# Optimization experiments

Measured on AMD Instinct MI355X. Metric: run time of the kernel, lower is better.

Reference implementation:

```python
import jax, jax.numpy as jnp
import numpy as np

N = 4096        # nodes (cells)
E = 131072      # edges (avg degree 32)
IN = 3000       # input features (genes)
HID = 128       # hidden dim per head
H = 4           # attention heads
LAT = 16        # latent dim
NEG_SLOPE = 0.2 # PyG GATConv leaky_relu slope


def _gat_sparse(x, src, dst, W, a_src, a_dst, b, concat):
    """PyG GATConv on an edge list (src -> dst, softmax grouped by dst)."""
    n = x.shape[0]
    h_, c = a_src.shape
    h = (x @ W).reshape(n, h_, c)                      # [N,H,C]
    e_src = (h * a_src[None]).sum(-1)                  # [N,H]
    e_dst = (h * a_dst[None]).sum(-1)                  # [N,H]
    e = jax.nn.leaky_relu(e_src[src] + e_dst[dst], NEG_SLOPE)  # [E,H]
    m = jax.ops.segment_max(e, dst, num_segments=n)
    ex = jnp.exp(e - m[dst])
    denom = jax.ops.segment_sum(ex, dst, num_segments=n)
    alpha = ex / (denom[dst] + 1e-16)                  # PyG softmax eps
    out = jax.ops.segment_sum(alpha[:, :, None] * h[src], dst, num_segments=n)
    out = out.reshape(n, h_ * c) if concat else out.mean(1)
    return out + b


def _gat_dense(x, W, a_src, a_dst, b, concat):
    """GATConv over the complete graph (the SVD low-rank reconstruction is
    generically fully dense, so to_sparse() keeps all N^2 entries; with
    used_edge_weight=False only the structure matters)."""
    n = x.shape[0]
    h_, c = a_src.shape
    h = (x @ W).reshape(n, h_, c)
    e_src = (h * a_src[None]).sum(-1)                  # [N,H]
    e_dst = (h * a_dst[None]).sum(-1)                  # [N,H]
    # scores[i (target), j (source), head]
    scores = jax.nn.leaky_relu(e_dst[:, None, :] + e_src[None, :, :], NEG_SLOPE)
    alpha = jax.nn.softmax(scores, axis=1)             # softmax over sources
    out = jnp.einsum('ijh,jhc->ihc', alpha, h)
    out = out.reshape(n, h_ * c) if concat else out.mean(1)
    return out + b


def setup_inputs() -> dict:
    key = jax.random.key(0)
    ks = jax.random.split(key, 16)
    s = 0.05
    x = jax.random.normal(ks[0], (N, IN), jnp.float32)
    src = jax.random.randint(ks[1], (E,), 0, N, jnp.int32)
    off = jax.random.randint(ks[2], (E,), 1, N, jnp.int32)
    dst = (src + off) % N                              # no self loops (PyG re-adds them)
    edge_index = jnp.stack([src, dst], axis=0)
    edge_attr = jax.random.uniform(ks[3], (E,), jnp.float32)
    D1 = H * HID
    return {
        'x': x, 'edge_index': edge_index, 'edge_attr': edge_attr,
        'W1': jax.random.normal(ks[4], (IN, D1), jnp.float32) * s,
        'a1_src': jax.random.normal(ks[5], (H, HID), jnp.float32) * s,
        'a1_dst': jax.random.normal(ks[6], (H, HID), jnp.float32) * s,
        'b1': jnp.zeros((D1,), jnp.float32),
        'Wm': jax.random.normal(ks[7], (D1, H * LAT), jnp.float32) * s,
        'am_src': jax.random.normal(ks[8], (H, LAT), jnp.float32) * s,
        'am_dst': jax.random.normal(ks[9], (H, LAT), jnp.float32) * s,
        'bm': jnp.zeros((LAT,), jnp.float32),
        'Ws': jax.random.normal(ks[10], (D1, H * LAT), jnp.float32) * s,
        'as_src': jax.random.normal(ks[11], (H, LAT), jnp.float32) * s,
        'as_dst': jax.random.normal(ks[12], (H, LAT), jnp.float32) * s,
        'bs': jnp.zeros((LAT,), jnp.float32),
    }


def reference(x, edge_index, edge_attr, W1, a1_src, a1_dst, b1,
              Wm, am_src, am_dst, bm, Ws, as_src, as_dst, bs):
    loops = jnp.arange(N, dtype=edge_index.dtype)
    src = jnp.concatenate([edge_index[0], loops])      # GATConv add_self_loops=True
    dst = jnp.concatenate([edge_index[1], loops])
    # branch 1: original sparse graph
    x1 = _gat_sparse(x, src, dst, W1, a1_src, a1_dst, b1, True)
    z_mean1 = _gat_sparse(x1, src, dst, Wm, am_src, am_dst, bm, False)
    z_log_std1 = _gat_sparse(x1, src, dst, Ws, as_src, as_dst, bs, False)
    # branch 2: SVD low-rank reconstructed adjacency => complete graph
    x2 = _gat_dense(x, W1, a1_src, a1_dst, b1, True)
    z_mean2 = _gat_dense(x2, Wm, am_src, am_dst, bm, False)
    z_log_std2 = _gat_dense(x2, Ws, as_src, as_dst, bs, False)
    return (z_mean1, z_log_std1, z_mean2, z_log_std2)
```

## Files before the change

kernel.cpp:

```cpp
#include <hip/hip_runtime.h>

typedef unsigned short u16;
typedef unsigned long long u64;
typedef __attribute__((ext_vector_type(8))) short short8;
typedef __attribute__((ext_vector_type(4))) float f32x4;

#define NN   4096
#define EE   131072
#define ETOT (EE + NN)
#define HH   4
#define IND  3000
#define KP   3008
#define D1   512
#define C1   128
#define C2   16

__device__ __forceinline__ float b2f(u16 u){
  union { unsigned int i; float f; } v; v.i = ((unsigned int)u) << 16; return v.f;
}
__device__ __forceinline__ u16 f2b(float f){
  unsigned int x = __float_as_uint(f);
  unsigned int r = (x + 0x7fffu + ((x >> 16) & 1u)) >> 16;
  return (u16)r;
}
__device__ __forceinline__ float lrelu(float x){ return x > 0.f ? x : 0.2f * x; }

__device__ __forceinline__ void glds16(const void* g, void* l){
  __builtin_amdgcn_global_load_lds(
      (const __attribute__((address_space(1))) unsigned int*)g,
      (__attribute__((address_space(3))) unsigned int*)l, 16, 0, 0);
}

__global__ void zero_out_kernel(float* p, int n){
  int i = blockIdx.x * blockDim.x + threadIdx.x;
  if (i < n) p[i] = 0.f;
}

__global__ __launch_bounds__(256) void cvtXW_kernel(const float* __restrict__ X,
    const float* __restrict__ W, u16* __restrict__ Xhi, u16* __restrict__ Xlo,
    u16* __restrict__ Whi, u16* __restrict__ Wlo){
  __shared__ float T[64][65];
  int b = blockIdx.x;
  if (b < 6016){
    int id = b * 256 + threadIdx.x;
    int m = id / 376, ch = id - m * 376;
    int k = ch * 8;
    float v[8];
    if (k + 8 <= IND){
      float4 a = *(const float4*)(X + (size_t)m * IND + k);
      float4 bb = *(const float4*)(X + (size_t)m * IND + k + 4);
      v[0]=a.x; v[1]=a.y; v[2]=a.z; v[3]=a.w; v[4]=bb.x; v[5]=bb.y; v[6]=bb.z; v[7]=bb.w;
    } else {
      #pragma unroll
      for (int j = 0; j < 8; ++j){ int kk = k + j; v[j] = (kk < IND) ? X[(size_t)m*IND + kk] : 0.f; }
    }
    u16 h8[8], l8[8];
    #pragma unroll
    for (int j = 0; j < 8; ++j){ h8[j] = f2b(v[j]); l8[j] = f2b(v[j] - b2f(h8[j])); }
    *(uint4*)(Xhi + (size_t)m * KP + k) = *(uint4*)h8;
    *(uint4*)(Xlo + (size_t)m * KP + k) = *(uint4*)l8;
  } else {
    int wb = b - 6016;
    int kb = wb % 47, nb = wb / 47;
    int k0 = kb * 64, n0 = nb * 64;
    int t = threadIdx.x;
    #pragma unroll
    for (int rr = 0; rr < 4; ++rr){
      int kl = (t >> 4) + rr * 16;
      int nn = (t & 15) * 4;
      int k = k0 + kl;
      float4 v = make_float4(0.f, 0.f, 0.f, 0.f);
      if (k < IND) v = *(const float4*)(W + (size_t)k * D1 + n0 + nn);
      T[kl][nn] = v.x; T[kl][nn+1] = v.y; T[kl][nn+2] = v.z; T[kl][nn+3] = v.w;
    }
    __syncthreads();
    int nloc = t >> 2, kseg = (t & 3) * 16;
    int n = n0 + nloc;
    #pragma unroll
    for (int c2 = 0; c2 < 2; ++c2){
      int kloc = kseg + c2 * 8;
      u16 h8[8], l8[8];
      #pragma unroll
      for (int j = 0; j < 8; ++j){
        float f = T[kloc + j][nloc];
        h8[j] = f2b(f); l8[j] = f2b(f - b2f(h8[j]));
      }
      *(uint4*)(Whi + (size_t)n * KP + k0 + kloc) = *(uint4*)h8;
      *(uint4*)(Wlo + (size_t)n * KP + k0 + kloc) = *(uint4*)l8;
    }
  }
}

__global__ __launch_bounds__(256) void cvtW2_kernel(const float* __restrict__ WM,
    const float* __restrict__ WS, u16* __restrict__ Wh, u16* __restrict__ Wl){
  __shared__ float T[64][65];
  int half = blockIdx.y;
  int k0 = blockIdx.x * 64;
  const float* W = half ? WS : WM;
  int t = threadIdx.x;
  #pragma unroll
  for (int p = 0; p < 4; ++p){
    int r = p * 16 + (t >> 4), c4 = (t & 15) * 4;
    float4 v = *(const float4*)(W + (size_t)(k0 + r) * 64 + c4);
    T[r][c4] = v.x; T[r][c4+1] = v.y; T[r][c4+2] = v.z; T[r][c4+3] = v.w;
  }
  __syncthreads();
  #pragma unroll
  for (int p = 0; p < 4; ++p){
    int n = p * 16 + (t >> 4), k4 = (t & 15) * 4;
    u16 h4[4], l4[4];
    #pragma unroll
    for (int j = 0; j < 4; ++j){
      float f = T[k4 + j][n];
      h4[j] = f2b(f); l4[j] = f2b(f - b2f(h4[j]));
    }
    size_t o = (size_t)(half * 64 + n) * 512 + k0 + k4;
    *(ushort4*)(Wh + o) = *(ushort4*)h4;
    *(ushort4*)(Wl + o) = *(ushort4*)l4;
  }
}

__global__ __launch_bounds__(256) void gemm_mfma(const u16* __restrict__ Xhi,
    const u16* __restrict__ Xlo, const u16* __restrict__ Whi, const u16* __restrict__ Wlo,
    float* __restrict__ Hh){
  __shared__ u16 sAh[64*64], sAl[64*64], sBh[64*64], sBl[64*64];
  int t = threadIdx.x, lane = t & 63;
  int wv = __builtin_amdgcn_readfirstlane(t >> 6);
  int wr = wv >> 1, wc = wv & 1;
  int bm = blockIdx.x * 64, bn = blockIdx.y * 64;
  f32x4 acc[2][2] = {};
  int r0 = t >> 3,         c0 = (t & 7) ^ (r0 & 7);
  int r1 = 32 + (t >> 3),  c1 = (t & 7) ^ (r1 & 7);
  const char* gAh0 = (const char*)(Xhi + (size_t)(bm + r0) * KP) + c0 * 16;
  const char* gAl0 = (const char*)(Xlo + (size_t)(bm + r0) * KP) + c0 * 16;
  const char* gAh1 = (const char*)(Xhi + (size_t)(bm + r1) * KP) + c1 * 16;
  const char* gAl1 = (const char*)(Xlo + (size_t)(bm + r1) * KP) + c1 * 16;
  const char* gBh0 = (const char*)(Whi + (size_t)(bn + r0) * KP) + c0 * 16;
  const char* gBl0 = (const char*)(Wlo + (size_t)(bn + r0) * KP) + c0 * 16;
  const char* gBh1 = (const char*)(Whi + (size_t)(bn + r1) * KP) + c1 * 16;
  const char* gBl1 = (const char*)(Wlo + (size_t)(bn + r1) * KP) + c1 * 16;
  char* lA0 = (char*)0 + t * 16;
  char* lA1 = (char*)0 + (t + 256) * 16;
  int r16 = lane & 15, kq = lane >> 4;
  int aoff[2][2], boff[2][2];
  #pragma unroll
  for (int m = 0; m < 2; ++m)
    #pragma unroll
    for (int ks = 0; ks < 2; ++ks){
      int arow = wr * 32 + m * 16 + r16;
      int cc = ks * 4 + kq;
      aoff[m][ks] = arow * 128 + ((cc ^ (arow & 7)) * 16);
    }
  #pragma unroll
  for (int n = 0; n < 2; ++n)
    #pragma unroll
    for (int ks = 0; ks < 2; ++ks){
      int brow = wc * 32 + n * 16 + r16;
      int cc = ks * 4 + kq;
      boff[n][ks] = brow * 128 + ((cc ^ (brow & 7)) * 16);
    }
  for (int kb = 0; kb < KP * 2; kb += 128){
    glds16(gAh0 + kb, (char*)sAh + (size_t)lA0);
    glds16(gAh1 + kb, (char*)sAh + (size_t)lA1);
    glds16(gAl0 + kb, (char*)sAl + (size_t)lA0);
    glds16(gAl1 + kb, (char*)sAl + (size_t)lA1);
    glds16(gBh0 + kb, (char*)sBh + (size_t)lA0);
    glds16(gBh1 + kb, (char*)sBh + (size_t)lA1);
    glds16(gBl0 + kb, (char*)sBl + (size_t)lA0);
    glds16(gBl1 + kb, (char*)sBl + (size_t)lA1);
    __syncthreads();
    #pragma unroll
    for (int ks = 0; ks < 2; ++ks){
      short8 ah[2], al[2], bh[2], bl[2];
      #pragma unroll
      for (int m = 0; m < 2; ++m){
        ah[m] = *(const short8*)((const char*)sAh + aoff[m][ks]);
        al[m] = *(const short8*)((const char*)sAl + aoff[m][ks]);
      }
      #pragma unroll
      for (int n = 0; n < 2; ++n){
        bh[n] = *(const short8*)((const char*)sBh + boff[n][ks]);
        bl[n] = *(const short8*)((const char*)sBl + boff[n][ks]);
      }
      #pragma unroll
      for (int m = 0; m < 2; ++m)
        #pragma unroll
        for (int n = 0; n < 2; ++n){
          acc[m][n] = __builtin_amdgcn_mfma_f32_16x16x32_bf16(ah[m], bh[n], acc[m][n], 0, 0, 0);
          acc[m][n] = __builtin_amdgcn_mfma_f32_16x16x32_bf16(ah[m], bl[n], acc[m][n], 0, 0, 0);
          acc[m][n] = __builtin_amdgcn_mfma_f32_16x16x32_bf16(al[m], bh[n], acc[m][n], 0, 0, 0);
        }
    }
    __syncthreads();
  }
  #pragma unroll
  for (int m = 0; m < 2; ++m)
    #pragma unroll
    for (int n = 0; n < 2; ++n){
      int row = bm + wr * 32 + m * 16 + kq * 4;
      int col = bn + wc * 32 + n * 16 + r16;
      float* o = Hh + (size_t)row * D1 + col;
      #pragma unroll
      for (int r = 0; r < 4; ++r) o[(size_t)r * D1] = acc[m][n][r];
    }
}

__global__ __launch_bounds__(256) void gemm_h_split(const float* __restrict__ X,
    const float* __restrict__ Wc, float* __restrict__ Hh){
  __shared__ u16 Ahs[64][40], Als[64][40], Bhs[64][40], Bls[64][40];
  int t = threadIdx.x, lane = t & 63, wave = t >> 6;
  int wr = wave >> 1, wcc = wave & 1;
  int bm = blockIdx.x * 64, bn = blockIdx.y * 64;
  f32x4 acc[2][2] = {};
  int arow = t >> 2, akc = (t & 3) << 3;
  int brow = t >> 3, bnc = (t & 7) << 3;
  for (int k0 = 0; k0 < IND; k0 += 32){
    float va[8];
    size_t abase = (size_t)(bm + arow) * IND + k0 + akc;
    if (k0 + akc + 8 <= IND){
      float4 r0 = *(const float4*)(X + abase);
      float4 r1 = *(const float4*)(X + abase + 4);
      va[0]=r0.x; va[1]=r0.y; va[2]=r0.z; va[3]=r0.w;
      va[4]=r1.x; va[5]=r1.y; va[6]=r1.z; va[7]=r1.w;
    } else {
      #pragma unroll
      for (int j = 0; j < 8; ++j){
        int k = k0 + akc + j;
        va[j] = (k < IND) ? X[abase + j] : 0.f;
      }
    }
    #pragma unroll
    for (int j = 0; j < 8; ++j){
      u16 hb = f2b(va[j]);
      Ahs[arow][akc + j] = hb;
      Als[arow][akc + j] = f2b(va[j] - b2f(hb));
    }
    {
      int gk = k0 + brow;
      float vb[8];
      if (gk < IND){
        const float* wp = Wc + (size_t)gk * D1 + bn + bnc;
        float4 r0 = *(const float4*)wp;
        float4 r1 = *(const float4*)(wp + 4);
        vb[0]=r0.x; vb[1]=r0.y; vb[2]=r0.z; vb[3]=r0.w;
        vb[4]=r1.x; vb[5]=r1.y; vb[6]=r1.z; vb[7]=r1.w;
      } else {
        #pragma unroll
        for (int j = 0; j < 8; ++j) vb[j] = 0.f;
      }
      #pragma unroll
      for (int j = 0; j < 8; ++j){
        u16 hb = f2b(vb[j]);
        Bhs[bnc + j][brow] = hb;
        Bls[bnc + j][brow] = f2b(vb[j] - b2f(hb));
      }
    }
    __syncthreads();
    int r16 = lane & 15, kq = (lane >> 4) << 3;
    short8 a0h = *(const short8*)&Ahs[wr*32      + r16][kq];
    short8 a1h = *(const short8*)&Ahs[wr*32 + 16 + r16][kq];
    short8 a0l = *(const short8*)&Als[wr*32      + r16][kq];
    short8 a1l = *(const short8*)&Als[wr*32 + 16 + r16][kq];
    short8 b0h = *(const short8*)&Bhs[wcc*32      + r16][kq];
    short8 b1h = *(const short8*)&Bhs[wcc*32 + 16 + r16][kq];
    short8 b0l = *(const short8*)&Bls[wcc*32      + r16][kq];
    short8 b1l = *(const short8*)&Bls[wcc*32 + 16 + r16][kq];
    acc[0][0] = __builtin_amdgcn_mfma_f32_16x16x32_bf16(a0h, b0h, acc[0][0], 0, 0, 0);
    acc[0][1] = __builtin_amdgcn_mfma_f32_16x16x32_bf16(a0h, b1h, acc[0][1], 0, 0, 0);
    acc[1][0] = __builtin_amdgcn_mfma_f32_16x16x32_bf16(a1h, b0h, acc[1][0], 0, 0, 0);
    acc[1][1] = __builtin_amdgcn_mfma_f32_16x16x32_bf16(a1h, b1h, acc[1][1], 0, 0, 0);
    acc[0][0] = __builtin_amdgcn_mfma_f32_16x16x32_bf16(a0h, b0l, acc[0][0], 0, 0, 0);
    acc[0][1] = __builtin_amdgcn_mfma_f32_16x16x32_bf16(a0h, b1l, acc[0][1], 0, 0, 0);
    acc[1][0] = __builtin_amdgcn_mfma_f32_16x16x32_bf16(a1h, b0l, acc[1][0], 0, 0, 0);
    acc[1][1] = __builtin_amdgcn_mfma_f32_16x16x32_bf16(a1h, b1l, acc[1][1], 0, 0, 0);
    acc[0][0] = __builtin_amdgcn_mfma_f32_16x16x32_bf16(a0l, b0h, acc[0][0], 0, 0, 0);
    acc[0][1] = __builtin_amdgcn_mfma_f32_16x16x32_bf16(a0l, b1h, acc[0][1], 0, 0, 0);
    acc[1][0] = __builtin_amdgcn_mfma_f32_16x16x32_bf16(a1l, b0h, acc[1][0], 0, 0, 0);
    acc[1][1] = __builtin_amdgcn_mfma_f32_16x16x32_bf16(a1l, b1h, acc[1][1], 0, 0, 0);
    __syncthreads();
  }
  int cr = (lane >> 4) << 2, cc = lane & 15;
  for (int i = 0; i < 2; ++i) for (int j = 0; j < 2; ++j){
    int row = bm + wr*32 + i*16 + cr;
    int col = bn + wcc*32 + j*16 + cc;
    float* o = Hh + (size_t)row * D1 + col;
    for (int r = 0; r < 4; ++r) o[(size_t)r * D1] = acc[i][j][r];
  }
}

__global__ __launch_bounds__(256) void transpose_h(const float* __restrict__ h,
    float* __restrict__ hT, u16* __restrict__ h16){
  __shared__ float T[64][65];
  int bm = blockIdx.x * 64, bc = blockIdx.y * 64;
  int t = threadIdx.x;
  #pragma unroll
  for (int p = 0; p < 4; ++p){
    int r = p * 16 + (t >> 4), c4 = (t & 15) * 4;
    float4 v = *(const float4*)(h + (size_t)(bm + r) * D1 + bc + c4);
    T[r][c4] = v.x; T[r][c4+1] = v.y; T[r][c4+2] = v.z; T[r][c4+3] = v.w;
    u16 q[4] = { f2b(v.x), f2b(v.y), f2b(v.z), f2b(v.w) };
    *(ushort4*)(h16 + (size_t)(bm + r) * D1 + bc + c4) = *(ushort4*)q;
  }
  __syncthreads();
  #pragma unroll
  for (int p = 0; p < 4; ++p){
    int c = p * 16 + (t >> 4), m4 = (t & 15) * 4;
    float4 o = make_float4(T[m4][c], T[m4+1][c], T[m4+2][c], T[m4+3][c]);
    *(float4*)(hT + (size_t)(bc + c) * NN + bm + m4) = o;
  }
}

__global__ __launch_bounds__(256) void evec128(const float* __restrict__ hsrc,
    const float* __restrict__ as_, const float* __restrict__ ad_,
    float* __restrict__ es, float* __restrict__ ed){
  int idx = blockIdx.x * 256 + threadIdx.x;
  if (idx >= NN * HH) return;
  int h = idx & 3;
  const float4* hp = (const float4*)(hsrc + (size_t)idx * C1);
  const float4* ap = (const float4*)(as_ + h * C1);
  const float4* dp = (const float4*)(ad_ + h * C1);
  float s1 = 0.f, s2 = 0.f;
  #pragma unroll
  for (int c = 0; c < 32; ++c){
    float4 v = hp[c], a = ap[c], d = dp[c];
    s1 += v.x*a.x + v.y*a.y + v.z*a.z + v.w*a.w;
    s2 += v.x*d.x + v.y*d.y + v.z*d.z + v.w*d.w;
  }
  es[idx] = s1; ed[idx] = s2;
}

__global__ void zero_kernel(int* p, int n){
  int i = blockIdx.x * blockDim.x + threadIdx.x;
  if (i < n) p[i] = 0;
}
__global__ void hist_kernel(const int* __restrict__ dstA, int* __restrict__ deg){
  int e = blockIdx.x * blockDim.x + threadIdx.x;
  if (e < ETOT){
    int d = (e < EE) ? dstA[e] : (e - EE);
    atomicAdd(&deg[d & (NN-1)], 1);
  }
}
__global__ __launch_bounds__(1024) void scan_kernel(const int* __restrict__ deg,
    int* __restrict__ off, int* __restrict__ cur){
  __shared__ int wsum[16];
  int t = threadIdx.x, lane = t & 63, wv = t >> 6;
  int v0 = deg[t*4], v1 = deg[t*4+1], v2 = deg[t*4+2], v3 = deg[t*4+3];
  int s = v0 + v1 + v2 + v3;
  int sc = s;
  #pragma unroll
  for (int o = 1; o < 64; o <<= 1){
    int y = __shfl_up(sc, o);
    if (lane >= o) sc += y;
  }
  if (lane == 63) wsum[wv] = sc;
  __syncthreads();
  int base = 0;
  #pragma unroll
  for (int i = 0; i < 16; ++i) base += (i < wv) ? wsum[i] : 0;
  int excl = base + sc - s;
  int a0 = excl, a1 = a0 + v0, a2 = a1 + v1, a3 = a2 + v2;
  off[t*4] = a0; off[t*4+1] = a1; off[t*4+2] = a2; off[t*4+3] = a3;
  cur[t*4] = a0; cur[t*4+1] = a1; cur[t*4+2] = a2; cur[t*4+3] = a3;
  if (t == 1023) off[4096] = base + sc;
}
__global__ void scatter_kernel(const int* __restrict__ srcA, const int* __restrict__ dstA,
    int* __restrict__ cur, int* __restrict__ sidx){
  int e = blockIdx.x * blockDim.x + threadIdx.x;
  if (e < ETOT){
    int s, d;
    if (e < EE){ s = srcA[e]; d = dstA[e]; } else { s = d = e - EE; }
    int pos = atomicAdd(&cur[d & (NN-1)], 1);
    pos = min(max(pos, 0), ETOT - 1);
    sidx[pos] = s & (NN-1);
  }
}

__global__ __launch_bounds__(256) void sparse1(const u16* __restrict__ h16,
    const float* __restrict__ es, const float* __restrict__ ed,
    const int* __restrict__ off, const int* __restrict__ sidx,
    const float* __restrict__ bias, u16* __restrict__ x1h, u16* __restrict__ x1l){
  int n = blockIdx.x, t = threadIdx.x, w = t >> 6;
  int o0 = off[n], deg = off[n+1] - o0;
  deg = min(max(deg, 0), ETOT);
  float edn = ed[n * HH + w];
  float dsum = 1e-16f, a0 = 0.f, a1 = 0.f;
  for (int e = 0; e < deg; ++e){
    int s = sidx[o0 + e] & (NN-1);
    float we = __expf(lrelu(es[s*HH + w] + edn));
    unsigned pk = *(const unsigned*)(h16 + ((size_t)s << 9) + 2*t);
    a0 = fmaf(we, b2f((u16)(pk & 0xffff)), a0);
    a1 = fmaf(we, b2f((u16)(pk >> 16)), a1);
    dsum += we;
  }
  float inv = 1.0f / dsum;
  float v0 = a0 * inv + bias[2*t];
  float v1 = a1 * inv + bias[2*t + 1];
  u16 h0 = f2b(v0), h1 = f2b(v1);
  u16 l0 = f2b(v0 - b2f(h0)), l1 = f2b(v1 - b2f(h1));
  size_t o = ((size_t)n << 9) + 2*t;
  *(unsigned*)(x1h + o) = (unsigned)h0 | ((unsigned)h1 << 16);
  *(unsigned*)(x1l + o) = (unsigned)l0 | ((unsigned)l1 << 16);
}

struct Sp2 { const float* h[2]; const float* es[2]; const float* ed[2];
             const float* bias[2]; float* out[2]; };
__global__ __launch_bounds__(64) void sparse2(Sp2 a,
    const int* __restrict__ off, const int* __restrict__ sidx){
  int n = blockIdx.x, sel = blockIdx.y;
  int lane = threadIdx.x, hh = lane >> 4;
  const float* hsrc = a.h[sel];
  const float* es = a.es[sel];
  const float* ed = a.ed[sel];
  int o0 = off[n], deg = off[n+1] - o0;
  deg = min(max(deg, 0), ETOT);
  float edn = ed[n * HH + hh];
  float dsum = 1e-16f, acc = 0.f;
  for (int e = 0; e < deg; ++e){
    int s = sidx[o0 + e] & (NN-1);
    float we = __expf(lrelu(es[s*HH + hh] + edn));
    acc = fmaf(we, hsrc[(size_t)s * 64 + lane], acc);
    dsum += we;
  }
  float v = acc / dsum;
  v += __shfl_xor(v, 16);
  v += __shfl_xor(v, 32);
  if (lane < 16) a.out[sel][(size_t)n * C2 + lane] = v * 0.25f + a.bias[sel][lane];
}

struct GsA {
  const u16* x1h; const u16* x1l; const u16* x2h; const u16* x2l;
  const u16* Wh; const u16* Wl;
  float* hm1; float* hs1; float* hm2T; float* hs2T;
  const float* AMS; const float* AMD; const float* ASS; const float* ASD;
  float* em1s; float* em1d; float* es1s; float* es1d;
  float* em2s; float* em2d; float* es2s; float* es2d;
};
__global__ __launch_bounds__(256) void gemm_small_fused(GsA a){
  __shared__ u16 sAh[32*64], sAl[32*64], sBh[128*64], sBl[128*64];
  int t = threadIdx.x, lane = t & 63;
  int wv = __builtin_amdgcn_readfirstlane(t >> 6);
  int src = blockIdx.y;
  int bm = blockIdx.x * 32;
  const u16* xh = src ? a.x2h : a.x1h;
  const u16* xl = src ? a.x2l : a.x1l;
  f32x4 acc[2][2] = {};
  int sarow = t >> 3, sac = (t & 7) ^ (sarow & 7);
  const char* gAh = (const char*)(xh + (size_t)(bm + sarow) * 512) + sac * 16;
  const char* gAl = (const char*)(xl + (size_t)(bm + sarow) * 512) + sac * 16;
  char* lAh = (char*)sAh + t * 16;
  char* lAl = (char*)sAl + t * 16;
  const char* gBh[4]; const char* gBl[4];
  #pragma unroll
  for (int q = 0; q < 4; ++q){
    int id = q * 256 + t;
    int br = id >> 3, bc = (id & 7) ^ (br & 7);
    gBh[q] = (const char*)(a.Wh + (size_t)br * 512) + bc * 16;
    gBl[q] = (const char*)(a.Wl + (size_t)br * 512) + bc * 16;
  }
  int r16 = lane & 15, kq = lane >> 4;
  int aoff[2][2], boff[2][2];
  #pragma unroll
  for (int m = 0; m < 2; ++m)
    #pragma unroll
    for (int ks = 0; ks < 2; ++ks){
      int arow = m * 16 + r16;
      int cc = ks * 4 + kq;
      aoff[m][ks] = arow * 128 + ((cc ^ (arow & 7)) * 16);
    }
  #pragma unroll
  for (int n = 0; n < 2; ++n)
    #pragma unroll
    for (int ks = 0; ks < 2; ++ks){
      int brow = wv * 32 + n * 16 + r16;
      int cc = ks * 4 + kq;
      boff[n][ks] = brow * 128 + ((cc ^ (brow & 7)) * 16);
    }
  for (int kb = 0; kb < 1024; kb += 128){
    glds16(gAh + kb, lAh);
    glds16(gAl + kb, lAl);
    #pragma unroll
    for (int q = 0; q < 4; ++q){
      glds16(gBh[q] + kb, (char*)sBh + (q * 256 + t) * 16);
      glds16(gBl[q] + kb, (char*)sBl + (q * 256 + t) * 16);
    }
    __syncthreads();
    #pragma unroll
    for (int ks = 0; ks < 2; ++ks){
      short8 ah[2], al[2], bh[2], bl[2];
      #pragma unroll
      for (int m = 0; m < 2; ++m){
        ah[m] = *(const short8*)((const char*)sAh + aoff[m][ks]);
        al[m] = *(const short8*)((const char*)sAl + aoff[m][ks]);
      }
      #pragma unroll
      for (int n = 0; n < 2; ++n){
        bh[n] = *(const short8*)((const char*)sBh + boff[n][ks]);
        bl[n] = *(const short8*)((const char*)sBl + boff[n][ks]);
      }
      #pragma unroll
      for (int m = 0; m < 2; ++m)
        #pragma unroll
        for (int n = 0; n < 2; ++n){
          acc[m][n] = __builtin_amdgcn_mfma_f32_16x16x32_bf16(ah[m], bh[n], acc[m][n], 0, 0, 0);
          acc[m][n] = __builtin_amdgcn_mfma_f32_16x16x32_bf16(ah[m], bl[n], acc[m][n], 0, 0, 0);
          acc[m][n] = __builtin_amdgcn_mfma_f32_16x16x32_bf16(al[m], bh[n], acc[m][n], 0, 0, 0);
        }
    }
    __syncthreads();
  }
  #pragma unroll
  for (int m = 0; m < 2; ++m){
    #pragma unroll
    for (int n = 0; n < 2; ++n){
      int colB = wv * 32 + n * 16;
      int half = colB >> 6;
      int colh = (colB & 63) + r16;
      int hh = (colB & 63) >> 4;
      int row0 = bm + m * 16 + kq * 4;
      if (src == 0){
        float* o = (half ? a.hs1 : a.hm1) + (size_t)row0 * 64 + colh;
        #pragma unroll
        for (int r = 0; r < 4; ++r) o[(size_t)r * 64] = acc[m][n][r];
      } else {
        float* oT = (half ? a.hs2T : a.hm2T) + (size_t)colh * NN + row0;
        *(float4*)oT = make_float4(acc[m][n][0], acc[m][n][1], acc[m][n][2], acc[m][n][3]);
      }
      const float* AS = half ? a.ASS : a.AMS;
      const float* AD = half ? a.ASD : a.AMD;
      float av = AS[colh], dv = AD[colh];
      float* esP = src ? (half ? a.es2s : a.em2s) : (half ? a.es1s : a.em1s);
      float* edP = src ? (half ? a.es2d : a.em2d) : (half ? a.es1d : a.em1d);
      #pragma unroll
      for (int r = 0; r < 4; ++r){
        float vs = acc[m][n][r] * av;
        float vd = acc[m][n][r] * dv;
        #pragma unroll
        for (int msk = 1; msk < 16; msk <<= 1){
          vs += __shfl_xor(vs, msk);
          vd += __shfl_xor(vd, msk);
        }
        if (r16 == 0){
          int rw = row0 + r;
          esP[rw * HH + hh] = vs;
          edP[rw * HH + hh] = vd;
        }
      }
    }
  }
}

struct RkA { const float* in[2]; float* us[2]; int* pm[2]; };
__global__ __launch_bounds__(1024) void rank_kernel(RkA a){
  int sid = blockIdx.y;
  int sel = sid >> 2, h = sid & 3;
  const float* evals = a.in[sel];
  __shared__ u64 K[NN];
  __shared__ int red[1024];
  int t = threadIdx.x;
  for (int i = t; i < NN; i += 1024){
    unsigned x = __float_as_uint(evals[i*HH + h]);
    x = (x & 0x80000000u) ? ~x : (x | 0x80000000u);
    K[i] = ((u64)x << 32) | (unsigned)i;
  }
  __syncthreads();
  int jl = t & 63, sp = t >> 6;
  int j = blockIdx.x * 64 + jl;
  u64 myk = K[j];
  int cnt = 0;
  int k0 = sp * 256;
  #pragma unroll 8
  for (int i = 0; i < 256; ++i)
    cnt += (K[k0 + i] < myk) ? 1 : 0;
  red[t] = cnt;
  __syncthreads();
  if (sp == 0){
    int rank = 0;
    #pragma unroll
    for (int s = 0; s < 16; ++s) rank += red[jl + 64*s];
    a.us[sel][h*NN + rank] = evals[j*HH + h];
    a.pm[sel][h*NN + rank] = j;
  }
}

struct PfxA { const float* T[2]; const int* pm[2]; const float* us[2];
              float* P1[2]; float* P2[2]; };
__global__ __launch_bounds__(512) void prefix_kernel(PfxA a, int C){
  int sel = blockIdx.y;
  int Cp = C + 1;
  int h = blockIdx.x / Cp, c = blockIdx.x % Cp;
  const float* Tsrc = a.T[sel];
  const int*   pm   = a.pm[sel] + h * NN;
  const float* us   = a.us[sel] + h * NN;
  float* P1 = a.P1[sel];
  float* P2 = a.P2[sel];
  const float* row = Tsrc + (size_t)(h * C + c) * NN;
  __shared__ float L1[NN], L2[NN];
  __shared__ float T1[8], T2[8], O1[9], O2[9];
  int t = threadIdx.x, lane = t & 63, w = t >> 6;
  size_t base = (size_t)h * (NN + 1);
  float run1 = 0.f, run2 = 0.f;
  for (int cc = 0; cc < 8; ++cc){
    int k = w * 512 + cc * 64 + lane;
    float u = us[k];
    float v = 1.0f;
    if (c < C){ int j = pm[k] & (NN-1); v = row[j]; }
    float t1 = __expf(u) * v;
    float t2 = __expf(0.2f * u) * v;
    float s1 = t1, s2 = t2;
    for (int o = 1; o < 64; o <<= 1){
      float y1 = __shfl_up(s1, o), y2 = __shfl_up(s2, o);
      if (lane >= o){ s1 += y1; s2 += y2; }
    }
    L1[k] = run1 + s1 - t1;
    L2[k] = run2 + s2 - t2;
    run1 += __shfl(s1, 63);
    run2 += __shfl(s2, 63);
  }
  if (lane == 63){ T1[w] = run1; T2[w] = run2; }
  __syncthreads();
  if (t == 0){
    float a1 = 0.f, a2 = 0.f;
    #pragma unroll
    for (int s = 0; s < 8; ++s){ O1[s] = a1; O2[s] = a2; a1 += T1[s]; a2 += T2[s]; }
    O1[8] = a1; O2[8] = a2;
  }
  __syncthreads();
  for (int i = t; i < NN; i += 512){
    P1[(base + i) * Cp + c] = L1[i] + O1[i >> 9];
    P2[(base + i) * Cp + c] = L2[i] + O2[i >> 9];
  }
  if (t == 0){
    P1[(base + NN) * Cp + c] = O1[8];
    P2[(base + NN) * Cp + c] = O2[8];
  }
}

template<int C, bool MEAN>
__device__ __forceinline__ void dense_body(const float* __restrict__ P1,
    const float* __restrict__ P2, const float* __restrict__ usort,
    const float* __restrict__ ed, const float* __restrict__ bias,
    float* __restrict__ outF, u16* __restrict__ outH, u16* __restrict__ outL, int i){
  constexpr int Cp = C + 1;
  constexpr int NC = HH * C;
  int t = threadIdx.x;
  __shared__ float Ed[HH], E2d[HH], Den[HH];
  __shared__ int   Kh[HH];
  __shared__ float vals[NC > 256 ? 1 : NC];
  if (t < HH){
    float d = ed[i*HH + t];
    float target = -d;
    const float* us = usort + t * NN;
    int lo = 0, hi = NN;
    while (lo < hi){ int mid = (lo + hi) >> 1; if (us[mid] < target) lo = mid + 1; else hi = mid; }
    Kh[t] = lo;
    float e1 = __expf(d), e2 = __expf(0.2f * d);
    Ed[t] = e1; E2d[t] = e2;
    size_t base = (size_t)t * (NN + 1);
    float p1N = P1[(base + NN) * Cp + C];
    float p1k = P1[(base + lo) * Cp + C];
    float p2k = P2[(base + lo) * Cp + C];
    Den[t] = e1 * (p1N - p1k) + e2 * p2k;
  }
  __syncthreads();
  if (!MEAN){
    for (int ch = t; ch < NC; ch += 256){
      int h = ch / C, c = ch % C;
      size_t base = (size_t)h * (NN + 1);
      float p1N = P1[(base + NN)    * Cp + c];
      float p1k = P1[(base + Kh[h]) * Cp + c];
      float p2k = P2[(base + Kh[h]) * Cp + c];
      float num = Ed[h] * (p1N - p1k) + E2d[h] * p2k;
      float val = num / Den[h] + bias[ch];
      u16 hb = f2b(val);
      outH[(size_t)i * NC + ch] = hb;
      outL[(size_t)i * NC + ch] = f2b(val - b2f(hb));
    }
  } else {
    if (t < NC){
      int h = t / C, c = t % C;
      size_t base = (size_t)h * (NN + 1);
      float p1N = P1[(base + NN)    * Cp + c];
      float p1k = P1[(base + Kh[h]) * Cp + c];
      float p2k = P2[(base + Kh[h]) * Cp + c];
      vals[t] = (Ed[h] * (p1N - p1k) + E2d[h] * p2k) / Den[h];
    }
    __syncthreads();
    if (t < C){
      float z = (vals[t] + vals[C + t] + vals[2*C + t] + vals[3*C + t]) * 0.25f + bias[t];
      outF[(size_t)i * C + t] = z;
    }
  }
}

__global__ __launch_bounds__(256) void dense_out1(const float* __restrict__ P1,
    const float* __restrict__ P2, const float* __restrict__ usort,
    const float* __restrict__ ed, const float* __restrict__ bias,
    u16* __restrict__ outH, u16* __restrict__ outL){
  dense_body<C1, false>(P1, P2, usort, ed, bias, nullptr, outH, outL, blockIdx.x);
}

struct Dn2 { const float* P1[2]; const float* P2[2]; const float* us[2];
             const float* ed[2]; const float* bias[2]; float* out[2]; };
__global__ __launch_bounds__(256) void dense_out2(Dn2 a){
  int s = blockIdx.y;
  dense_body<C2, true>(a.P1[s], a.P2[s], a.us[s], a.ed[s], a.bias[s], a.out[s],
                       nullptr, nullptr, blockIdx.x);
}

extern "C" void kernel_launch(void* const* d_in, const int* in_sizes, int n_in,
                              void* d_out, int out_size, void* d_ws, size_t ws_size,
                              hipStream_t stream){
  const float* X   = (const float*)d_in[0];
  const int*   EI  = (const int*)d_in[1];
  const float* W1  = (const float*)d_in[3];
  const float* A1S = (const float*)d_in[4];
  const float* A1D = (const float*)d_in[5];
  const float* B1  = (const float*)d_in[6];
  const float* WM  = (const float*)d_in[7];
  const float* AMS = (const float*)d_in[8];
  const float* AMD = (const float*)d_in[9];
  const float* BM  = (const float*)d_in[10];
  const float* WS  = (const float*)d_in[11];
  const float* ASS = (const float*)d_in[12];
  const float* ASD = (const float*)d_in[13];
  const float* BS  = (const float*)d_in[14];
  float* OUT = (float*)d_out;
  (void)in_sizes; (void)n_in;

  if (ws_size < (size_t)56 * 1024 * 1024){
    zero_out_kernel<<<dim3((out_size + 255)/256), 256, 0, stream>>>(OUT, out_size);
    return;
  }
  bool fast = (ws_size >= (size_t)68 * 1024 * 1024);

  const size_t MB = 1024 * 1024;
  char* w = (char*)d_ws;
  size_t o = 0;
  auto alloc = [&](size_t bytes) -> void* {
    void* p = w + o;
    o += (bytes + 255) & ~(size_t)255;
    return p;
  };
  int*   deg  = (int*)  alloc(NN * 4);
  int*   coff = (int*)  alloc((NN + 1) * 4);
  int*   cur  = (int*)  alloc(NN * 4);
  int*   sidx = (int*)  alloc((size_t)ETOT * 4);
  float* e1s  = (float*)alloc(NN * HH * 4);
  float* e1d  = (float*)alloc(NN * HH * 4);
  float* us1  = (float*)alloc(HH * NN * 4);
  int*   pm1  = (int*)  alloc(HH * NN * 4);
  float* em1s = (float*)alloc(NN * HH * 4);
  float* em1d = (float*)alloc(NN * HH * 4);
  float* es1s = (float*)alloc(NN * HH * 4);
  float* es1d = (float*)alloc(NN * HH * 4);
  float* em2s = (float*)alloc(NN * HH * 4);
  float* em2d = (float*)alloc(NN * HH * 4);
  float* es2s = (float*)alloc(NN * HH * 4);
  float* es2d = (float*)alloc(NN * HH * 4);
  float* us2m = (float*)alloc(HH * NN * 4);
  int*   pm2m = (int*)  alloc(HH * NN * 4);
  float* us2s = (float*)alloc(HH * NN * 4);
  int*   pm2s = (int*)  alloc(HH * NN * 4);
  u16*   Wh2  = (u16*)  alloc(128 * 512 * 2);
  u16*   Wl2  = (u16*)  alloc(128 * 512 * 2);
  float* h    = (float*)alloc((size_t)NN * D1 * 4);
  char*  BIG  = w + o;
  size_t szX = (size_t)NN * KP * 2, szW = (size_t)D1 * KP * 2;
  u16* Xhi = (u16*)BIG;
  u16* Xlo = (u16*)(BIG + szX);
  u16* Whi = (u16*)(BIG + 2*szX);
  u16* Wlo = (u16*)(BIG + 2*szX + szW);
  u16*   x1h = (u16*)  (BIG + 0*MB);
  u16*   x1l = (u16*)  (BIG + 4*MB);
  u16*   x2h = (u16*)  (BIG + 8*MB);
  u16*   x2l = (u16*)  (BIG + 12*MB);
  float* hT  = (float*)(BIG + 16*MB);
  u16*   h16 = (u16*)  (BIG + 24*MB);
  float* P1a = (float*)(BIG + 28*MB);
  float* P2a = (float*)(BIG + 37*MB);
  float* hm1  = (float*)(BIG + 16*MB);
  float* hs1  = (float*)(BIG + 17*MB);
  float* hm2T = (float*)(BIG + 18*MB);
  float* hs2T = (float*)(BIG + 19*MB);
  float* P1m  = (float*)(BIG + 20*MB);
  float* P2m  = (float*)(BIG + 21*MB + 512*1024);
  float* P1s  = (float*)(BIG + 23*MB);
  float* P2s  = (float*)(BIG + 24*MB + 512*1024);

  const int* srcA = EI;
  const int* dstA = EI + EE;

  cvtW2_kernel<<<dim3(8, 2), 256, 0, stream>>>(WM, WS, Wh2, Wl2);
  if (fast){
    cvtXW_kernel<<<dim3(6016 + 47*8), 256, 0, stream>>>(X, W1, Xhi, Xlo, Whi, Wlo);
    gemm_mfma<<<dim3(NN/64, D1/64), 256, 0, stream>>>(Xhi, Xlo, Whi, Wlo, h);
  } else {
    gemm_h_split<<<dim3(NN/64, D1/64), 256, 0, stream>>>(X, W1, h);
  }
  transpose_h<<<dim3(NN/64, D1/64), 256, 0, stream>>>(h, hT, h16);
  evec128<<<dim3(NN*HH/256), 256, 0, stream>>>(h, A1S, A1D, e1s, e1d);
  zero_kernel<<<dim3(16), 256, 0, stream>>>(deg, NN);
  hist_kernel<<<dim3((ETOT + 255)/256), 256, 0, stream>>>(dstA, deg);
  scan_kernel<<<dim3(1), 1024, 0, stream>>>(deg, coff, cur);
  scatter_kernel<<<dim3((ETOT + 255)/256), 256, 0, stream>>>(srcA, dstA, cur, sidx);
  sparse1<<<dim3(NN), 256, 0, stream>>>(h16, e1s, e1d, coff, sidx, B1, x1h, x1l);
  {
    RkA ra; ra.in[0] = e1s; ra.in[1] = e1s; ra.us[0] = us1; ra.us[1] = us1;
    ra.pm[0] = pm1; ra.pm[1] = pm1;
    rank_kernel<<<dim3(64, 4), 1024, 0, stream>>>(ra);
    PfxA pa; pa.T[0] = hT; pa.T[1] = hT; pa.pm[0] = pm1; pa.pm[1] = pm1;
    pa.us[0] = us1; pa.us[1] = us1; pa.P1[0] = P1a; pa.P1[1] = P1a;
    pa.P2[0] = P2a; pa.P2[1] = P2a;
    prefix_kernel<<<dim3(HH*(C1+1), 1), 512, 0, stream>>>(pa, C1);
    dense_out1<<<dim3(NN), 256, 0, stream>>>(P1a, P2a, us1, e1d, B1, x2h, x2l);
  }
  {
    GsA ga;
    ga.x1h = x1h; ga.x1l = x1l; ga.x2h = x2h; ga.x2l = x2l;
    ga.Wh = Wh2; ga.Wl = Wl2;
    ga.hm1 = hm1; ga.hs1 = hs1; ga.hm2T = hm2T; ga.hs2T = hs2T;
    ga.AMS = AMS; ga.AMD = AMD; ga.ASS = ASS; ga.ASD = ASD;
    ga.em1s = em1s; ga.em1d = em1d; ga.es1s = es1s; ga.es1d = es1d;
    ga.em2s = em2s; ga.em2d = em2d; ga.es2s = es2s; ga.es2d = es2d;
    gemm_small_fused<<<dim3(NN/32, 2), 256, 0, stream>>>(ga);
  }
  {
    Sp2 sp;
    sp.h[0] = hm1; sp.h[1] = hs1; sp.es[0] = em1s; sp.es[1] = es1s;
    sp.ed[0] = em1d; sp.ed[1] = es1d; sp.bias[0] = BM; sp.bias[1] = BS;
    sp.out[0] = OUT; sp.out[1] = OUT + (size_t)NN*C2;
    sparse2<<<dim3(NN, 2), 64, 0, stream>>>(sp, coff, sidx);
  }
  {
    RkA ra; ra.in[0] = em2s; ra.in[1] = es2s; ra.us[0] = us2m; ra.us[1] = us2s;
    ra.pm[0] = pm2m; ra.pm[1] = pm2s;
    rank_kernel<<<dim3(64, 8), 1024, 0, stream>>>(ra);
    PfxA pa; pa.T[0] = hm2T; pa.T[1] = hs2T; pa.pm[0] = pm2m; pa.pm[1] = pm2s;
    pa.us[0] = us2m; pa.us[1] = us2s; pa.P1[0] = P1m; pa.P1[1] = P1s;
    pa.P2[0] = P2m; pa.P2[1] = P2s;
    prefix_kernel<<<dim3(HH*(C2+1), 2), 512, 0, stream>>>(pa, C2);
    Dn2 dn;
    dn.P1[0] = P1m; dn.P1[1] = P1s; dn.P2[0] = P2m; dn.P2[1] = P2s;
    dn.us[0] = us2m; dn.us[1] = us2s; dn.ed[0] = em2d; dn.ed[1] = es2d;
    dn.bias[0] = BM; dn.bias[1] = BS;
    dn.out[0] = OUT + (size_t)2*NN*C2; dn.out[1] = OUT + (size_t)3*NN*C2;
    dense_out2<<<dim3(NN, 2), 256, 0, stream>>>(dn);
  }
}
```

Measured before the change: 393.4 us.

## Split K across two wave groups in gemm_mfma with LDS reduction

The first-layer MFMA GEMM goes from 256 to 512 threads per block. The 8 waves form two groups that each take half of the 64-wide K chunk, and their partial accumulators are summed through shared memory at the end. Each thread now issues one async global-to-LDS load per matrix instead of two. The goal is more waves per tile to hide latency, at the cost of a final reduction, an extra barrier and higher per-block resource use.

```diff
diff --git a/kernel.cpp b/kernel.cpp
--- a/kernel.cpp
+++ b/kernel.cpp
@@ -120,89 +120,97 @@
   }
 }
 
-__global__ __launch_bounds__(256) void gemm_mfma(const u16* __restrict__ Xhi,
+__global__ __launch_bounds__(512) void gemm_mfma(const u16* __restrict__ Xhi,
     const u16* __restrict__ Xlo, const u16* __restrict__ Whi, const u16* __restrict__ Wlo,
     float* __restrict__ Hh){
-  __shared__ u16 sAh[64*64], sAl[64*64], sBh[64*64], sBl[64*64];
+  __shared__ char smem[32768];
+  u16* sAh = (u16*)smem;
+  u16* sAl = (u16*)(smem + 8192);
+  u16* sBh = (u16*)(smem + 16384);
+  u16* sBl = (u16*)(smem + 24576);
   int t = threadIdx.x, lane = t & 63;
   int wv = __builtin_amdgcn_readfirstlane(t >> 6);
-  int wr = wv >> 1, wc = wv & 1;
+  int ksw = wv >> 2;
+  int wr = (wv >> 1) & 1, wc = wv & 1;
   int bm = blockIdx.x * 64, bn = blockIdx.y * 64;
   f32x4 acc[2][2] = {};
-  int r0 = t >> 3,         c0 = (t & 7) ^ (r0 & 7);
-  int r1 = 32 + (t >> 3),  c1 = (t & 7) ^ (r1 & 7);
-  const char* gAh0 = (const char*)(Xhi + (size_t)(bm + r0) * KP) + c0 * 16;
-  const char* gAl0 = (const char*)(Xlo + (size_t)(bm + r0) * KP) + c0 * 16;
-  const char* gAh1 = (const char*)(Xhi + (size_t)(bm + r1) * KP) + c1 * 16;
-  const char* gAl1 = (const char*)(Xlo + (size_t)(bm + r1) * KP) + c1 * 16;
-  const char* gBh0 = (const char*)(Whi + (size_t)(bn + r0) * KP) + c0 * 16;
-  const char* gBl0 = (const char*)(Wlo + (size_t)(bn + r0) * KP) + c0 * 16;
-  const char* gBh1 = (const char*)(Whi + (size_t)(bn + r1) * KP) + c1 * 16;
-  const char* gBl1 = (const char*)(Wlo + (size_t)(bn + r1) * KP) + c1 * 16;
-  char* lA0 = (char*)0 + t * 16;
-  char* lA1 = (char*)0 + (t + 256) * 16;
+  int srow = t >> 3;
+  int sc = (t & 7) ^ (srow & 7);
+  const char* gAh = (const char*)(Xhi + (size_t)(bm + srow) * KP) + sc * 16;
+  const char* gAl = (const char*)(Xlo + (size_t)(bm + srow) * KP) + sc * 16;
+  const char* gBh = (const char*)(Whi + (size_t)(bn + srow) * KP) + sc * 16;
+  const char* gBl = (const char*)(Wlo + (size_t)(bn + srow) * KP) + sc * 16;
+  char* lAh = (char*)sAh + t * 16;
+  char* lAl = (char*)sAl + t * 16;
+  char* lBh = (char*)sBh + t * 16;
+  char* lBl = (char*)sBl + t * 16;
   int r16 = lane & 15, kq = lane >> 4;
-  int aoff[2][2], boff[2][2];
-  #pragma unroll
-  for (int m = 0; m < 2; ++m)
-    #pragma unroll
-    for (int ks = 0; ks < 2; ++ks){
-      int arow = wr * 32 + m * 16 + r16;
-      int cc = ks * 4 + kq;
-      aoff[m][ks] = arow * 128 + ((cc ^ (arow & 7)) * 16);
-    }
-  #pragma unroll
-  for (int n = 0; n < 2; ++n)
-    #pragma unroll
-    for (int ks = 0; ks < 2; ++ks){
-      int brow = wc * 32 + n * 16 + r16;
-      int cc = ks * 4 + kq;
-      boff[n][ks] = brow * 128 + ((cc ^ (brow & 7)) * 16);
-    }
+  int cc = ksw * 4 + kq;
+  int aoff[2], boff[2];
+  #pragma unroll
+  for (int m = 0; m < 2; ++m){
+    int arow = wr * 32 + m * 16 + r16;
+    aoff[m] = arow * 128 + ((cc ^ (arow & 7)) * 16);
+  }
+  #pragma unroll
+  for (int n = 0; n < 2; ++n){
+    int brow = wc * 32 + n * 16 + r16;
+    boff[n] = brow * 128 + ((cc ^ (brow & 7)) * 16);
+  }
   for (int kb = 0; kb < KP * 2; kb += 128){
-    glds16(gAh0 + kb, (char*)sAh + (size_t)lA0);
-    glds16(gAh1 + kb, (char*)sAh + (size_t)lA1);
-    glds16(gAl0 + kb, (char*)sAl + (size_t)lA0);
-    glds16(gAl1 + kb, (char*)sAl + (size_t)lA1);
-    glds16(gBh0 + kb, (char*)sBh + (size_t)lA0);
-    glds16(gBh1 + kb, (char*)sBh + (size_t)lA1);
-    glds16(gBl0 + kb, (char*)sBl + (size_t)lA0);
-    glds16(gBl1 + kb, (char*)sBl + (size_t)lA1);
+    glds16(gAh + kb, lAh);
+    glds16(gAl + kb, lAl);
+    glds16(gBh + kb, lBh);
+    glds16(gBl + kb, lBl);
     __syncthreads();
-    #pragma unroll
-    for (int ks = 0; ks < 2; ++ks){
-      short8 ah[2], al[2], bh[2], bl[2];
-      #pragma unroll
-      for (int m = 0; m < 2; ++m){
-        ah[m] = *(const short8*)((const char*)sAh + aoff[m][ks]);
-        al[m] = *(const short8*)((const char*)sAl + aoff[m][ks]);
-      }
+    short8 ah[2], al[2], bh[2], bl[2];
+    #pragma unroll
+    for (int m = 0; m < 2; ++m){
+      ah[m] = *(const short8*)((const char*)sAh + aoff[m]);
+      al[m] = *(const short8*)((const char*)sAl + aoff[m]);
+    }
+    #pragma unroll
+    for (int n = 0; n < 2; ++n){
+      bh[n] = *(const short8*)((const char*)sBh + boff[n]);
+      bl[n] = *(const short8*)((const char*)sBl + boff[n]);
+    }
+    #pragma unroll
+    for (int m = 0; m < 2; ++m)
       #pragma unroll
       for (int n = 0; n < 2; ++n){
-        bh[n] = *(const short8*)((const char*)sBh + boff[n][ks]);
-        bl[n] = *(const short8*)((const char*)sBl + boff[n][ks]);
-      }
-      #pragma unroll
-      for (int m = 0; m < 2; ++m)
+        acc[m][n] = __builtin_amdgcn_mfma_f32_16x16x32_bf16(ah[m], bh[n], acc[m][n], 0, 0, 0);
+        acc[m][n] = __builtin_amdgcn_mfma_f32_16x16x32_bf16(ah[m], bl[n], acc[m][n], 0, 0, 0);
+        acc[m][n] = __builtin_amdgcn_mfma_f32_16x16x32_bf16(al[m], bh[n], acc[m][n], 0, 0, 0);
+      }
+    __syncthreads();
+  }
+  float* red = (float*)smem;
+  int pp = wr * 2 + wc;
+  if (ksw){
+    #pragma unroll
+    for (int m = 0; m < 2; ++m)
+      #pragma unroll
+      for (int n = 0; n < 2; ++n)
         #pragma unroll
-        for (int n = 0; n < 2; ++n){
-          acc[m][n] = __builtin_amdgcn_mfma_f32_16x16x32_bf16(ah[m], bh[n], acc[m][n], 0, 0, 0);
-          acc[m][n] = __builtin_amdgcn_mfma_f32_16x16x32_bf16(ah[m], bl[n], acc[m][n], 0, 0, 0);
-          acc[m][n] = __builtin_amdgcn_mfma_f32_16x16x32_bf16(al[m], bh[n], acc[m][n], 0, 0, 0);
-        }
-    }
-    __syncthreads();
-  }
-  #pragma unroll
-  for (int m = 0; m < 2; ++m)
-    #pragma unroll
-    for (int n = 0; n < 2; ++n){
-      int row = bm + wr * 32 + m * 16 + kq * 4;
-      int col = bn + wc * 32 + n * 16 + r16;
-      float* o = Hh + (size_t)row * D1 + col;
-      #pragma unroll
-      for (int r = 0; r < 4; ++r) o[(size_t)r * D1] = acc[m][n][r];
-    }
+        for (int r = 0; r < 4; ++r)
+          red[((((m*2+n)*4 + r) << 8) + (pp << 6)) + lane] = acc[m][n][r];
+  }
+  __syncthreads();
+  if (!ksw){
+    #pragma unroll
+    for (int m = 0; m < 2; ++m)
+      #pragma unroll
+      for (int n = 0; n < 2; ++n){
+        #pragma unroll
+        for (int r = 0; r < 4; ++r)
+          acc[m][n][r] += red[((((m*2+n)*4 + r) << 8) + (pp << 6)) + lane];
+        int row = bm + wr * 32 + m * 16 + kq * 4;
+        int col = bn + wc * 32 + n * 16 + r16;
+        float* o = Hh + (size_t)row * D1 + col;
+        #pragma unroll
+        for (int r = 0; r < 4; ++r) o[(size_t)r * D1] = acc[m][n][r];
+      }
+  }
 }
 
 __global__ __launch_bounds__(256) void gemm_h_split(const float* __restrict__ X,
@@ -793,7 +801,7 @@
   cvtW2_kernel<<<dim3(8, 2), 256, 0, stream>>>(WM, WS, Wh2, Wl2);
   if (fast){
     cvtXW_kernel<<<dim3(6016 + 47*8), 256, 0, stream>>>(X, W1, Xhi, Xlo, Whi, Wlo);
-    gemm_mfma<<<dim3(NN/64, D1/64), 256, 0, stream>>>(Xhi, Xlo, Whi, Wlo, h);
+    gemm_mfma<<<dim3(NN/64, D1/64), 512, 0, stream>>>(Xhi, Xlo, Whi, Wlo, h);
   } else {
     gemm_h_split<<<dim3(NN/64, D1/64), 256, 0, stream>>>(X, W1, h);
   }
```

New measurement: 387.5 us. No clear change (-1.5%).
